# Kernel tuning notes

Hardware: AMD Instinct MI355X
Metric: run time of the kernel (lower is better)

## Reference

```python
import jax, jax.numpy as jnp
import numpy as np

B, S, H, NH, L, FF, V, T = 16, 256, 768, 12, 12, 3072, 30522, 9
DH = H // NH
LN_EPS = 1e-12


def _ln(x, g, b):
    m = jnp.mean(x, axis=-1, keepdims=True)
    v = jnp.mean((x - m) ** 2, axis=-1, keepdims=True)
    return (x - m) * jax.lax.rsqrt(v + LN_EPS) * g + b


def setup_inputs():
    key = jax.random.key(0)
    ks = jax.random.split(key, 20)
    n = lambda i, shape: jax.random.normal(ks[i], shape, jnp.float32) * 0.02
    lengths = jax.random.randint(ks[0], (B,), S // 2, S + 1)
    attention_mask = (jnp.arange(S)[None, :] < lengths[:, None]).astype(jnp.int32)
    return {
        "input_ids": jax.random.randint(ks[1], (B, S), 0, V),
        "attention_mask": attention_mask,
        "labels": jax.random.randint(ks[2], (B, S), 0, T),
        "word_emb": n(3, (V, H)),
        "pos_emb": n(4, (512, H)),
        "type_emb": n(5, (2, H)),
        "emb_g": jnp.ones((H,), jnp.float32), "emb_b": jnp.zeros((H,), jnp.float32),
        "lWq": n(6, (L, H, H)), "lbq": jnp.zeros((L, H), jnp.float32),
        "lWk": n(7, (L, H, H)), "lbk": jnp.zeros((L, H), jnp.float32),
        "lWv": n(8, (L, H, H)), "lbv": jnp.zeros((L, H), jnp.float32),
        "lWo": n(9, (L, H, H)), "lbo": jnp.zeros((L, H), jnp.float32),
        "lg1": jnp.ones((L, H), jnp.float32), "lb1": jnp.zeros((L, H), jnp.float32),
        "lWi": n(10, (L, H, FF)), "lbi": jnp.zeros((L, FF), jnp.float32),
        "lWf": n(11, (L, FF, H)), "lbf": jnp.zeros((L, H), jnp.float32),
        "lg2": jnp.ones((L, H), jnp.float32), "lb2": jnp.zeros((L, H), jnp.float32),
        "cls_W": n(12, (H, T)), "cls_b": jnp.zeros((T,), jnp.float32),
        "crf_start": jax.random.uniform(ks[13], (T,), jnp.float32, -0.1, 0.1),
        "crf_end": jax.random.uniform(ks[14], (T,), jnp.float32, -0.1, 0.1),
        "crf_trans": jax.random.uniform(ks[15], (T, T), jnp.float32, -0.1, 0.1),
    }


def _encoder(input_ids, attention_mask, word_emb, pos_emb, type_emb, emb_g, emb_b, layer_stack, cls_W, cls_b):
    x = word_emb[input_ids] + pos_emb[:S][None] + type_emb[0][None, None]  # [B,S,H]
    x = _ln(x, emb_g, emb_b)
    bias = (1.0 - attention_mask.astype(jnp.float32))[:, None, None, :] * -1e9  # [B,1,1,S]
    scale = 1.0 / np.sqrt(DH).astype(np.float32)

    def layer(h, p):
        Wq, bq, Wk, bk, Wv, bv, Wo, bo, g1, b1, Wi, bi, Wf, bf, g2, b2 = p
        q = (h @ Wq + bq).reshape(B, S, NH, DH)
        k = (h @ Wk + bk).reshape(B, S, NH, DH)
        v = (h @ Wv + bv).reshape(B, S, NH, DH)
        att = jax.nn.softmax(jnp.einsum('bqhd,bkhd->bhqk', q, k) * scale + bias, axis=-1)
        ctx = jnp.einsum('bhqk,bkhd->bqhd', att, v).reshape(B, S, H)
        h = _ln(h + ctx @ Wo + bo, g1, b1)
        ff = jax.nn.gelu(h @ Wi + bi, approximate=False) @ Wf + bf
        h = _ln(h + ff, g2, b2)
        return h, None

    x, _ = jax.lax.scan(layer, x, layer_stack)
    return x @ cls_W + cls_b  # [B,S,T]


def _crf_llh(em, tg, m, start, end, trans):
    # pytorch-crf forward, reduction='sum'. em [B,Lc,T], tg [B,Lc] int, m [B,Lc] bool
    mf = m.astype(em.dtype)
    em_sc = jnp.take_along_axis(em, tg[..., None], axis=-1)[..., 0]  # [B,Lc]
    tr_sc = trans[tg[:, :-1], tg[:, 1:]]                             # [B,Lc-1]
    num = start[tg[:, 0]] + em_sc[:, 0] + jnp.sum(mf[:, 1:] * (tr_sc + em_sc[:, 1:]), axis=1)
    seq_ends = jnp.sum(m.astype(jnp.int32), axis=1) - 1
    last_tag = jnp.take_along_axis(tg, seq_ends[:, None], axis=1)[:, 0]
    num = num + end[last_tag]

    def step(score, xs):
        em_t, m_t = xs
        nxt = jax.nn.logsumexp(score[:, :, None] + trans[None] + em_t[:, None, :], axis=1)
        return jnp.where(m_t[:, None], nxt, score), None

    score0 = start[None] + em[:, 0]
    score, _ = jax.lax.scan(step, score0, (em[:, 1:].transpose(1, 0, 2), m[:, 1:].transpose(1, 0)))
    den = jax.nn.logsumexp(score + end[None], axis=1)
    return jnp.sum(num - den)


def _viterbi(em, start, end, trans):
    # decode over the FULL sequence with all-ones mask (matches crf.decode(logits))
    def step(score, em_t):
        cand = score[:, :, None] + trans[None] + em_t[:, None, :]  # [B,T,T]
        return jnp.max(cand, axis=1), jnp.argmax(cand, axis=1)

    score0 = start[None] + em[:, 0]
    score, hist = jax.lax.scan(step, score0, em[:, 1:].transpose(1, 0, 2))  # hist [S-1,B,T]
    last = jnp.argmax(score + end[None], axis=1)  # [B]

    def back(tag, h):
        prev = jnp.take_along_axis(h, tag[:, None], axis=1)[:, 0]
        return prev, prev

    _, rev = jax.lax.scan(back, last, hist, reverse=True)  # rev[i] = tag at time i, i in [0,S-2]
    tags = jnp.concatenate([rev.transpose(1, 0), last[:, None]], axis=1)  # [B,S]
    return tags.astype(jnp.float32)


def reference(input_ids, attention_mask, labels, word_emb, pos_emb, type_emb, emb_g, emb_b,
              lWq, lbq, lWk, lbk, lWv, lbv, lWo, lbo, lg1, lb1, lWi, lbi, lWf, lbf, lg2, lb2,
              cls_W, cls_b, crf_start, crf_end, crf_trans):
    layer_stack = (lWq, lbq, lWk, lbk, lWv, lbv, lWo, lbo, lg1, lb1, lWi, lbi, lWf, lbf, lg2, lb2)
    logits = _encoder(input_ids, attention_mask, word_emb, pos_emb, type_emb, emb_g, emb_b, layer_stack, cls_W, cls_b)
    str_lens = jnp.sum(attention_mask, axis=-1)
    pos = jnp.arange(S)[None, :]
    mask = attention_mask.astype(bool) & (pos > 0) & (pos != (str_lens - 1)[:, None])
    tags_in = jnp.where(mask, labels, jnp.zeros_like(labels))
    loss = -_crf_llh(logits[:, 1:], tags_in[:, 1:], mask[:, 1:], crf_start, crf_end, crf_trans)
    tags = _viterbi(logits, crf_start, crf_end, crf_trans)
    return (loss, tags)
```

## Files before the change

### kernel.cpp

```cpp
#include <hip/hip_runtime.h>

#define B_ 16
#define S_ 256
#define H_ 768
#define NH_ 12
#define DH_ 64
#define L_ 12
#define FF_ 3072
#define T_ 9
#define NTOK (B_*S_)

typedef __attribute__((ext_vector_type(8))) short bfrag;
typedef __attribute__((ext_vector_type(8))) unsigned short us8;
typedef __attribute__((ext_vector_type(4))) float f4;

__device__ inline unsigned short f2bf(float x) {
    unsigned u = __builtin_bit_cast(unsigned, x);
    return (unsigned short)((u + 0x7fffu + ((u >> 16) & 1u)) >> 16);
}
__device__ inline float bf2f(unsigned short h) {
    unsigned u = ((unsigned)h) << 16;
    return __builtin_bit_cast(float, u);
}
__device__ inline void pack8(const float* v, us8& h, us8& l) {
    #pragma unroll
    for (int j = 0; j < 8; j++) {
        unsigned short hh = f2bf(v[j]);
        h[j] = hh;
        l[j] = f2bf(v[j] - bf2f(hh));
    }
}

__global__ __launch_bounds__(256) void k_conv_w(
    const float* __restrict__ Wq, const float* __restrict__ Wk,
    const float* __restrict__ Wv, const float* __restrict__ Wo,
    const float* __restrict__ Wi, const float* __restrict__ Wf,
    const float* __restrict__ bq, const float* __restrict__ bk, const float* __restrict__ bv,
    float* __restrict__ qkvbias, unsigned short* __restrict__ Wpk)
{
    int bid = blockIdx.x;
    int tid = threadIdx.x;
    if (bid == 0) {
        for (int i = tid; i < 3 * H_; i += 256)
            qkvbias[i] = (i < H_) ? bq[i] : (i < 2 * H_) ? bk[i - H_] : bv[i - 2 * H_];
    }
    const float* src; int Kd, Nd; size_t doff; int t;
    if (bid < 576)       { int m = bid / 144; src = (m == 0) ? Wq : (m == 1) ? Wk : (m == 2) ? Wv : Wo;
                           Kd = H_; Nd = H_; doff = (size_t)m * 73728; t = bid % 144; }
    else if (bid < 1152) { src = Wi; Kd = H_; Nd = FF_; doff = 294912; t = bid - 576; }
    else                 { src = Wf; Kd = FF_; Nd = H_; doff = 589824; t = bid - 1152; }
    int ntn = Nd / 64;
    int tk = t / ntn, tn = t % ntn;
    int k0 = tk * 64, n0 = tn * 64;
    __shared__ float tile[64][65];
    int r = tid >> 6, c = tid & 63;
    #pragma unroll
    for (int i = 0; i < 16; i++)
        tile[r + i * 4][c] = src[(size_t)(k0 + r + i * 4) * Nd + n0 + c];
    __syncthreads();
    #pragma unroll
    for (int e = 0; e < 2; e++) {
        int item = tid * 2 + e;
        int nl = item >> 3, kb = item & 7;
        float v8[8];
        #pragma unroll
        for (int j = 0; j < 8; j++) v8[j] = tile[kb * 8 + j][nl];
        us8 h, l; pack8(v8, h, l);
        unsigned short* p = Wpk + (doff + (size_t)(n0 + nl) * (Kd / 8) + (k0 / 8 + kb)) * 16;
        *reinterpret_cast<us8*>(p) = h;
        *reinterpret_cast<us8*>(p + 8) = l;
    }
}

__global__ __launch_bounds__(128) void k_embed_ln(
    const int* __restrict__ ids, const float* __restrict__ wemb,
    const float* __restrict__ pemb, const float* __restrict__ temb,
    const float* __restrict__ g, const float* __restrict__ bb,
    float* __restrict__ out, unsigned short* __restrict__ out_pk)
{
    int tok = blockIdx.x;
    int s = tok & (S_ - 1);
    int id = ids[tok];
    int tid = threadIdx.x;
    bool act = tid < 96;
    int idx = tid * 8;
    float v8[8];
    float sum = 0.f;
    if (act) {
        const float4* w4 = reinterpret_cast<const float4*>(wemb + (size_t)id * H_ + idx);
        const float4* p4 = reinterpret_cast<const float4*>(pemb + (size_t)s * H_ + idx);
        const float4* t4 = reinterpret_cast<const float4*>(temb + idx);
        #pragma unroll
        for (int q = 0; q < 2; q++) {
            float4 a = w4[q], b = p4[q], c = t4[q];
            v8[q*4+0] = a.x + b.x + c.x; v8[q*4+1] = a.y + b.y + c.y;
            v8[q*4+2] = a.z + b.z + c.z; v8[q*4+3] = a.w + b.w + c.w;
        }
        #pragma unroll
        for (int j = 0; j < 8; j++) sum += v8[j];
    }
    __shared__ float wsum[2], wvar[2];
    #pragma unroll
    for (int o = 32; o > 0; o >>= 1) sum += __shfl_xor(sum, o);
    if ((tid & 63) == 0) wsum[tid >> 6] = sum;
    __syncthreads();
    float mean = (wsum[0] + wsum[1]) * (1.0f / H_);
    float vs = 0.f;
    if (act) {
        for (int j = 0; j < 8; j++) { float d = v8[j] - mean; vs += d * d; }
    }
    #pragma unroll
    for (int o = 32; o > 0; o >>= 1) vs += __shfl_xor(vs, o);
    if ((tid & 63) == 0) wvar[tid >> 6] = vs;
    __syncthreads();
    float inv = 1.0f / sqrtf((wvar[0] + wvar[1]) * (1.0f / H_) + 1e-12f);
    if (act) {
        float o8[8];
        #pragma unroll
        for (int j = 0; j < 8; j++) o8[j] = (v8[j] - mean) * inv * g[idx + j] + bb[idx + j];
        float4* d4 = reinterpret_cast<float4*>(out + (size_t)tok * H_ + idx);
        d4[0] = make_float4(o8[0], o8[1], o8[2], o8[3]);
        d4[1] = make_float4(o8[4], o8[5], o8[6], o8[7]);
        us8 h, l; pack8(o8, h, l);
        unsigned short* p = out_pk + ((size_t)tok * 96 + tid) * 16;
        *reinterpret_cast<us8*>(p) = h;
        *reinterpret_cast<us8*>(p + 8) = l;
    }
}

__global__ __launch_bounds__(128) void k_res_ln(
    const float* __restrict__ x, const float* __restrict__ res,
    const float* __restrict__ g, const float* __restrict__ bb,
    float* __restrict__ out, unsigned short* __restrict__ out_pk)
{
    int tok = blockIdx.x;
    int tid = threadIdx.x;
    bool act = tid < 96;
    int idx = tid * 8;
    float v8[8];
    float sum = 0.f;
    if (act) {
        const float4* x4 = reinterpret_cast<const float4*>(x + (size_t)tok * H_ + idx);
        const float4* r4 = reinterpret_cast<const float4*>(res + (size_t)tok * H_ + idx);
        #pragma unroll
        for (int q = 0; q < 2; q++) {
            float4 a = x4[q], b = r4[q];
            v8[q*4+0] = a.x + b.x; v8[q*4+1] = a.y + b.y;
            v8[q*4+2] = a.z + b.z; v8[q*4+3] = a.w + b.w;
        }
        #pragma unroll
        for (int j = 0; j < 8; j++) sum += v8[j];
    }
    __shared__ float wsum[2], wvar[2];
    #pragma unroll
    for (int o = 32; o > 0; o >>= 1) sum += __shfl_xor(sum, o);
    if ((tid & 63) == 0) wsum[tid >> 6] = sum;
    __syncthreads();
    float mean = (wsum[0] + wsum[1]) * (1.0f / H_);
    float vs = 0.f;
    if (act) {
        for (int j = 0; j < 8; j++) { float d = v8[j] - mean; vs += d * d; }
    }
    #pragma unroll
    for (int o = 32; o > 0; o >>= 1) vs += __shfl_xor(vs, o);
    if ((tid & 63) == 0) wvar[tid >> 6] = vs;
    __syncthreads();
    float inv = 1.0f / sqrtf((wvar[0] + wvar[1]) * (1.0f / H_) + 1e-12f);
    if (act) {
        float o8[8];
        #pragma unroll
        for (int j = 0; j < 8; j++) o8[j] = (v8[j] - mean) * inv * g[idx + j] + bb[idx + j];
        float4* d4 = reinterpret_cast<float4*>(out + (size_t)tok * H_ + idx);
        d4[0] = make_float4(o8[0], o8[1], o8[2], o8[3]);
        d4[1] = make_float4(o8[4], o8[5], o8[6], o8[7]);
        us8 h, l; pack8(o8, h, l);
        unsigned short* p = out_pk + ((size_t)tok * 96 + tid) * 16;
        *reinterpret_cast<us8*>(p) = h;
        *reinterpret_cast<us8*>(p + 8) = l;
    }
}

__global__ __launch_bounds__(256) void k_gemm_pk(
    const unsigned short* __restrict__ A, const unsigned short* __restrict__ Wp,
    const float* __restrict__ bias,
    float* __restrict__ C0, float* __restrict__ C1, float* __restrict__ C2, int cpb,
    unsigned short* __restrict__ Cpk,
    int M, int N, int K, int act)
{
    __shared__ char smem[32768];
    char* smA = smem;
    char* smB = smem + 16384;

    int nbx = N >> 7;
    int nwg = (M >> 7) * nbx;
    int id = blockIdx.x;
    int cpx = nwg >> 3;
    int swz = (id & 7) * cpx + (id >> 3);
    int by = swz / nbx, bx = swz % nbx;
    int m0 = by << 7, n0 = bx << 7;
    int Kb = K >> 3;
    int nst = Kb >> 2;

    int tid = threadIdx.x;
    int lane = tid & 63, wid = tid >> 6;
    int wm = wid >> 1, wn = wid & 1;
    int fr = lane & 15, fq = lane >> 4;

    f4 acc[4][4];
    #pragma unroll
    for (int i = 0; i < 4; i++)
        #pragma unroll
        for (int j = 0; j < 4; j++) acc[i][j] = (f4){0.f, 0.f, 0.f, 0.f};

    const char* agp[4]; const char* bgp[4];
    int alds[4];
    #pragma unroll
    for (int i = 0; i < 4; i++) {
        int off = i * 4096 + tid * 16;
        int row = off >> 7, col = off & 127;
        agp[i] = (const char*)A + (size_t)(m0 + row) * (Kb * 32) + col;
        bgp[i] = (const char*)Wp + (size_t)(n0 + row) * (Kb * 32) + col;
        alds[i] = row * 128 + (col ^ ((row & 7) << 4));
    }

    int arow = wm * 64 + fr;
    int brow = wn * 64 + fr;
    int afo[4], bfo[4];
    #pragma unroll
    for (int mi = 0; mi < 4; mi++) {
        int r = arow + mi * 16;
        afo[mi] = r * 128 + ((fq * 32) ^ ((r & 7) << 4));
        int rb = brow + mi * 16;
        bfo[mi] = rb * 128 + ((fq * 32) ^ ((rb & 7) << 4));
    }

    us8 ra[4], rb[4];
    #pragma unroll
    for (int i = 0; i < 4; i++) {
        ra[i] = *reinterpret_cast<const us8*>(agp[i]);
        rb[i] = *reinterpret_cast<const us8*>(bgp[i]);
    }

    for (int ks = 0; ks < nst; ks++) {
        #pragma unroll
        for (int i = 0; i < 4; i++) {
            *reinterpret_cast<us8*>(smA + alds[i]) = ra[i];
            *reinterpret_cast<us8*>(smB + alds[i]) = rb[i];
        }
        __syncthreads();
        if (ks + 1 < nst) {
            #pragma unroll
            for (int i = 0; i < 4; i++) {
                ra[i] = *reinterpret_cast<const us8*>(agp[i] + (size_t)(ks + 1) * 128);
                rb[i] = *reinterpret_cast<const us8*>(bgp[i] + (size_t)(ks + 1) * 128);
            }
        }
        bfrag ah[4], al[4], bh[4], bl[4];
        #pragma unroll
        for (int mi = 0; mi < 4; mi++) {
            ah[mi] = *reinterpret_cast<const bfrag*>(smA + afo[mi]);
            al[mi] = *reinterpret_cast<const bfrag*>(smA + (afo[mi] ^ 16));
            bh[mi] = *reinterpret_cast<const bfrag*>(smB + bfo[mi]);
            bl[mi] = *reinterpret_cast<const bfrag*>(smB + (bfo[mi] ^ 16));
        }
        #pragma unroll
        for (int mi = 0; mi < 4; mi++) {
            #pragma unroll
            for (int ni = 0; ni < 4; ni++) {
                acc[mi][ni] = __builtin_amdgcn_mfma_f32_16x16x32_bf16(ah[mi], bh[ni], acc[mi][ni], 0, 0, 0);
                acc[mi][ni] = __builtin_amdgcn_mfma_f32_16x16x32_bf16(ah[mi], bl[ni], acc[mi][ni], 0, 0, 0);
                acc[mi][ni] = __builtin_amdgcn_mfma_f32_16x16x32_bf16(al[mi], bh[ni], acc[mi][ni], 0, 0, 0);
            }
        }
        __syncthreads();
    }

    if (act == 0) {
        #pragma unroll
        for (int mi = 0; mi < 4; mi++) {
            #pragma unroll
            for (int ni = 0; ni < 4; ni++) {
                int col = n0 + wn * 64 + ni * 16 + fr;
                float bv = bias[col];
                int buf = col / cpb;
                float* Cp = (buf == 0) ? C0 : (buf == 1) ? C1 : C2;
                int cc = col - buf * cpb;
                #pragma unroll
                for (int r = 0; r < 4; r++) {
                    int row = m0 + wm * 64 + mi * 16 + fq * 4 + r;
                    Cp[(size_t)row * cpb + cc] = acc[mi][ni][r] + bv;
                }
            }
        }
    } else {
        float* ebuf = (float*)smem;
        int Nb = N >> 3;
        #pragma unroll
        for (int mi = 0; mi < 4; mi++) {
            #pragma unroll
            for (int ni = 0; ni < 4; ni++) {
                int col = n0 + wn * 64 + ni * 16 + fr;
                float bv = bias[col];
                #pragma unroll
                for (int r = 0; r < 4; r++) {
                    float v = acc[mi][ni][r] + bv;
                    v = 0.5f * v * (1.0f + erff(v * 0.70710678118654752f));
                    ebuf[(wid * 16 + fq * 4 + r) * 68 + ni * 16 + fr] = v;
                }
            }
            #pragma unroll
            for (int e = 0; e < 2; e++) {
                int item = lane * 2 + e;
                int row16 = item >> 3, kb = item & 7;
                float v8[8];
                #pragma unroll
                for (int j = 0; j < 8; j++) v8[j] = ebuf[(wid * 16 + row16) * 68 + kb * 8 + j];
                us8 h, l; pack8(v8, h, l);
                int grow = m0 + wm * 64 + mi * 16 + row16;
                int gcb = ((n0 + wn * 64) >> 3) + kb;
                unsigned short* p = Cpk + ((size_t)grow * Nb + gcb) * 16;
                *reinterpret_cast<us8*>(p) = h;
                *reinterpret_cast<us8*>(p + 8) = l;
            }
        }
    }
}

#define SM_KH 0
#define SM_KL 5632
#define SM_VH 11264
#define SM_VL 16384
#define SM_PH 21504
#define SM_PL 26624
__global__ __launch_bounds__(256) void k_attn_fused(
    const float* __restrict__ Q, const float* __restrict__ Kb,
    const float* __restrict__ V, const int* __restrict__ amask,
    unsigned short* __restrict__ ctx_pk)
{
    __shared__ char smem[31744];
    unsigned short* KhS = (unsigned short*)(smem + SM_KH);
    unsigned short* KlS = (unsigned short*)(smem + SM_KL);
    unsigned short* VhS = (unsigned short*)(smem + SM_VH);
    unsigned short* VlS = (unsigned short*)(smem + SM_VL);
    unsigned short* PhS = (unsigned short*)(smem + SM_PH);
    unsigned short* PlS = (unsigned short*)(smem + SM_PL);

    int idx = blockIdx.x;
    int qt = idx & 3;
    int hd = (idx >> 2) % NH_;
    int b = idx / (4 * NH_);
    int tid = threadIdx.x;
    int lane = tid & 63, wid = tid >> 6;
    int fr = lane & 15, fq = lane >> 4;

    int q0 = qt * 64 + wid * 16;

    bfrag qh[2], ql[2];
    {
        const float* qbase = Q + ((size_t)(b * S_ + q0 + fr)) * H_ + hd * DH_;
        #pragma unroll
        for (int ks = 0; ks < 2; ks++) {
            const float4* p = reinterpret_cast<const float4*>(qbase + ks * 32 + fq * 8);
            float4 v0 = p[0], v1 = p[1];
            float vv[8] = {v0.x, v0.y, v0.z, v0.w, v1.x, v1.y, v1.z, v1.w};
            #pragma unroll
            for (int j = 0; j < 8; j++) {
                unsigned short h = f2bf(vv[j]);
                qh[ks][j] = (short)h;
                ql[ks][j] = (short)f2bf(vv[j] - bf2f(h));
            }
        }
    }

    f4 o[4];
    #pragma unroll
    for (int i = 0; i < 4; i++) o[i] = (f4){0.f, 0.f, 0.f, 0.f};
    float m[4], l[4];
    #pragma unroll
    for (int r = 0; r < 4; r++) { m[r] = -3e38f; l[r] = 0.f; }

    int kvrow = tid >> 3;
    int dbase = (tid & 7) * 8;

    for (int t = 0; t < 8; t++) {
        {
            const float* src = Kb + ((size_t)(b * S_ + t * 32 + kvrow)) * H_ + hd * DH_ + dbase;
            float4 a4 = reinterpret_cast<const float4*>(src)[0];
            float4 b4 = reinterpret_cast<const float4*>(src)[1];
            float vv[8] = {a4.x, a4.y, a4.z, a4.w, b4.x, b4.y, b4.z, b4.w};
            us8 h, l2;
            #pragma unroll
            for (int j = 0; j < 8; j++) {
                unsigned short hh = f2bf(vv[j]);
                h[j] = hh; l2[j] = f2bf(vv[j] - bf2f(hh));
            }
            *reinterpret_cast<us8*>(&KhS[kvrow * 88 + dbase]) = h;
            *reinterpret_cast<us8*>(&KlS[kvrow * 88 + dbase]) = l2;
        }
        {
            const float* src = V + ((size_t)(b * S_ + t * 32 + kvrow)) * H_ + hd * DH_ + dbase;
            float4 a4 = reinterpret_cast<const float4*>(src)[0];
            float4 b4 = reinterpret_cast<const float4*>(src)[1];
            float vv[8] = {a4.x, a4.y, a4.z, a4.w, b4.x, b4.y, b4.z, b4.w};
            #pragma unroll
            for (int j = 0; j < 8; j++) {
                unsigned short h = f2bf(vv[j]);
                VhS[(dbase + j) * 40 + kvrow] = h;
                VlS[(dbase + j) * 40 + kvrow] = f2bf(vv[j] - bf2f(h));
            }
        }
        __syncthreads();

        f4 s0 = (f4){0.f,0.f,0.f,0.f}, s1 = (f4){0.f,0.f,0.f,0.f};
        #pragma unroll
        for (int ks = 0; ks < 2; ks++) {
            bfrag kbh0 = *reinterpret_cast<const bfrag*>(&KhS[fr * 88 + ks * 32 + fq * 8]);
            bfrag kbl0 = *reinterpret_cast<const bfrag*>(&KlS[fr * 88 + ks * 32 + fq * 8]);
            bfrag kbh1 = *reinterpret_cast<const bfrag*>(&KhS[(16 + fr) * 88 + ks * 32 + fq * 8]);
            bfrag kbl1 = *reinterpret_cast<const bfrag*>(&KlS[(16 + fr) * 88 + ks * 32 + fq * 8]);
            s0 = __builtin_amdgcn_mfma_f32_16x16x32_bf16(qh[ks], kbh0, s0, 0, 0, 0);
            s0 = __builtin_amdgcn_mfma_f32_16x16x32_bf16(qh[ks], kbl0, s0, 0, 0, 0);
            s0 = __builtin_amdgcn_mfma_f32_16x16x32_bf16(ql[ks], kbh0, s0, 0, 0, 0);
            s1 = __builtin_amdgcn_mfma_f32_16x16x32_bf16(qh[ks], kbh1, s1, 0, 0, 0);
            s1 = __builtin_amdgcn_mfma_f32_16x16x32_bf16(qh[ks], kbl1, s1, 0, 0, 0);
            s1 = __builtin_amdgcn_mfma_f32_16x16x32_bf16(ql[ks], kbh1, s1, 0, 0, 0);
        }

        float cb0 = (amask[b * S_ + t * 32 + fr] == 0) ? -1e9f : 0.f;
        float cb1 = (amask[b * S_ + t * 32 + 16 + fr] == 0) ? -1e9f : 0.f;
        float sc0[4], sc1[4], fct[4], pr0[4], pr1[4];
        #pragma unroll
        for (int r = 0; r < 4; r++) {
            sc0[r] = s0[r] * 0.125f + cb0;
            sc1[r] = s1[r] * 0.125f + cb1;
            float tm = fmaxf(sc0[r], sc1[r]);
            #pragma unroll
            for (int od = 1; od < 16; od <<= 1) tm = fmaxf(tm, __shfl_xor(tm, od));
            float mn = fmaxf(m[r], tm);
            fct[r] = expf(m[r] - mn);
            pr0[r] = expf(sc0[r] - mn);
            pr1[r] = expf(sc1[r] - mn);
            float rs = pr0[r] + pr1[r];
            #pragma unroll
            for (int od = 1; od < 16; od <<= 1) rs += __shfl_xor(rs, od);
            l[r] = l[r] * fct[r] + rs;
            m[r] = mn;
        }
        #pragma unroll
        for (int ci = 0; ci < 4; ci++)
            #pragma unroll
            for (int r = 0; r < 4; r++) o[ci][r] *= fct[r];

        #pragma unroll
        for (int r = 0; r < 4; r++) {
            int row = fq * 4 + r;
            unsigned short h0 = f2bf(pr0[r]);
            PhS[wid * 640 + row * 40 + fr] = h0;
            PlS[wid * 640 + row * 40 + fr] = f2bf(pr0[r] - bf2f(h0));
            unsigned short h1 = f2bf(pr1[r]);
            PhS[wid * 640 + row * 40 + 16 + fr] = h1;
            PlS[wid * 640 + row * 40 + 16 + fr] = f2bf(pr1[r] - bf2f(h1));
        }

        bfrag pah = *reinterpret_cast<const bfrag*>(&PhS[wid * 640 + fr * 40 + fq * 8]);
        bfrag pal = *reinterpret_cast<const bfrag*>(&PlS[wid * 640 + fr * 40 + fq * 8]);
        #pragma unroll
        for (int ci = 0; ci < 4; ci++) {
            bfrag vbh = *reinterpret_cast<const bfrag*>(&VhS[(ci * 16 + fr) * 40 + fq * 8]);
            bfrag vbl = *reinterpret_cast<const bfrag*>(&VlS[(ci * 16 + fr) * 40 + fq * 8]);
            o[ci] = __builtin_amdgcn_mfma_f32_16x16x32_bf16(pah, vbh, o[ci], 0, 0, 0);
            o[ci] = __builtin_amdgcn_mfma_f32_16x16x32_bf16(pah, vbl, o[ci], 0, 0, 0);
            o[ci] = __builtin_amdgcn_mfma_f32_16x16x32_bf16(pal, vbh, o[ci], 0, 0, 0);
        }
        __syncthreads();
    }

    __syncthreads();
    float* eb = (float*)smem + wid * 1088;
    #pragma unroll
    for (int r = 0; r < 4; r++) {
        float inv = 1.0f / l[r];
        #pragma unroll
        for (int ci = 0; ci < 4; ci++)
            eb[(fq * 4 + r) * 68 + ci * 16 + fr] = o[ci][r] * inv;
    }
    __syncthreads();
    #pragma unroll
    for (int e = 0; e < 2; e++) {
        int item = lane * 2 + e;
        int row16 = item >> 3, kb = item & 7;
        float v8[8];
        #pragma unroll
        for (int j = 0; j < 8; j++) v8[j] = eb[row16 * 68 + kb * 8 + j];
        us8 h, l2; pack8(v8, h, l2);
        int grow = b * S_ + q0 + row16;
        int gcb = hd * 8 + kb;
        unsigned short* p = ctx_pk + ((size_t)grow * 96 + gcb) * 16;
        *reinterpret_cast<us8*>(p) = h;
        *reinterpret_cast<us8*>(p + 8) = l2;
    }
}

__global__ __launch_bounds__(64) void k_classifier(
    const float* __restrict__ Hs, const float* __restrict__ Wc,
    const float* __restrict__ bc, float* __restrict__ logits)
{
    int tok = blockIdx.x;
    int lane = threadIdx.x;
    const float* hr = Hs + (size_t)tok * H_;
    float acc[T_];
    #pragma unroll
    for (int j = 0; j < T_; j++) acc[j] = 0.f;
    for (int k = lane; k < H_; k += 64) {
        float hv = hr[k];
        const float* wr = Wc + (size_t)k * T_;
        #pragma unroll
        for (int j = 0; j < T_; j++) acc[j] = fmaf(hv, wr[j], acc[j]);
    }
    #pragma unroll
    for (int j = 0; j < T_; j++) {
        float v = acc[j];
        for (int o = 32; o > 0; o >>= 1) v += __shfl_down(v, o);
        if (lane == 0) logits[(size_t)tok * T_ + j] = v + bc[j];
    }
}

__global__ __launch_bounds__(256) void k_crf(
    const float* __restrict__ logits, const int* __restrict__ amask,
    const int* __restrict__ labels, const float* __restrict__ start,
    const float* __restrict__ endv, const float* __restrict__ trans,
    float* __restrict__ out_loss)
{
    __shared__ float res[B_];
    int tid = threadIdx.x;
    int lane = tid & 63;
    int g = lane >> 4;
    int bb = (tid >> 6) * 4 + g;
    int sj = lane & 15;
    int lb = lane & 48;

    int cnt = 0;
    for (int s = sj; s < S_; s += 16) cnt += amask[bb * S_ + s];
    #pragma unroll
    for (int o = 8; o > 0; o >>= 1) cnt += __shfl_xor(cnt, o);
    int len = cnt;

    float num = 0.f; int msum = 0;
    for (int s = 2 + sj; s < S_; s += 16) {
        int mk = (amask[bb * S_ + s] != 0) && (s != len - 1);
        if (mk) {
            int sp = s - 1;
            int mkp = (amask[bb * S_ + sp] != 0) && (sp != len - 1) && (sp > 0);
            int tp = mkp ? labels[bb * S_ + sp] : 0;
            int tc = labels[bb * S_ + s];
            num += trans[tp * T_ + tc] + logits[((size_t)(bb * S_ + s)) * T_ + tc];
            msum++;
        }
    }
    #pragma unroll
    for (int o = 8; o > 0; o >>= 1) { num += __shfl_xor(num, o); msum += __shfl_xor(msum, o); }
    int mk1 = (amask[bb * S_ + 1] != 0) && (1 != len - 1);
    msum += mk1 ? 1 : 0;
    int tg1 = mk1 ? labels[bb * S_ + 1] : 0;
    num += start[tg1] + logits[((size_t)(bb * S_ + 1)) * T_ + tg1];
    int ls = msum;
    int mkl = (amask[bb * S_ + ls] != 0) && (ls != len - 1) && (ls > 0);
    num += endv[mkl ? labels[bb * S_ + ls] : 0];

    float tc9[T_];
    #pragma unroll
    for (int i = 0; i < T_; i++) tc9[i] = 0.f;
    if (sj < T_) {
        #pragma unroll
        for (int i = 0; i < T_; i++) tc9[i] = trans[i * T_ + sj];
    }
    float score = (sj < T_) ? start[sj] + logits[((size_t)(bb * S_ + 1)) * T_ + sj] : 0.f;
    for (int s = 2; s < S_; s++) {
        float em = (sj < T_) ? logits[((size_t)(bb * S_ + s)) * T_ + sj] : 0.f;
        float si[T_];
        #pragma unroll
        for (int i = 0; i < T_; i++) si[i] = __shfl(score, lb + i);
        int mt = (amask[bb * S_ + s] != 0) && (s != len - 1);
        float mx = -1e30f;
        #pragma unroll
        for (int i = 0; i < T_; i++) mx = fmaxf(mx, si[i] + tc9[i]);
        float sum = 0.f;
        #pragma unroll
        for (int i = 0; i < T_; i++) sum += expf(si[i] + tc9[i] - mx);
        float nsc = mx + logf(sum) + em;
        if (mt) score = nsc;
    }

    float se = (sj < T_) ? score + endv[sj] : -1e30f;
    float fi[T_];
    #pragma unroll
    for (int i = 0; i < T_; i++) fi[i] = __shfl(se, lb + i);
    if (sj == 0) {
        float mx = -1e30f;
        #pragma unroll
        for (int i = 0; i < T_; i++) mx = fmaxf(mx, fi[i]);
        float sum = 0.f;
        #pragma unroll
        for (int i = 0; i < T_; i++) sum += expf(fi[i] - mx);
        res[bb] = (mx + logf(sum)) - num;
    }
    __syncthreads();
    if (tid == 0) {
        float tot = 0.f;
        #pragma unroll
        for (int i = 0; i < B_; i++) tot += res[i];
        out_loss[0] = tot;
    }
}

__global__ __launch_bounds__(64) void k_viterbi(
    const float* __restrict__ logits, const float* __restrict__ start,
    const float* __restrict__ endv, const float* __restrict__ trans,
    float* __restrict__ tags_out)
{
    int b = blockIdx.x;
    int j = threadIdx.x;
    __shared__ unsigned char hist[S_ - 1][T_];
    float tc9[T_];
    #pragma unroll
    for (int i = 0; i < T_; i++) tc9[i] = 0.f;
    if (j < T_) {
        #pragma unroll
        for (int i = 0; i < T_; i++) tc9[i] = trans[i * T_ + j];
    }
    float score = (j < T_) ? start[j] + logits[((size_t)(b * S_)) * T_ + j] : -1e30f;
    for (int t = 1; t < S_; t++) {
        float si[T_];
        #pragma unroll
        for (int i = 0; i < T_; i++) si[i] = __shfl(score, i);
        float best = -1e30f; int bi = 0;
        #pragma unroll
        for (int i = 0; i < T_; i++) {
            float c = si[i] + tc9[i];
            if (c > best) { best = c; bi = i; }
        }
        if (j < T_) {
            hist[t - 1][j] = (unsigned char)bi;
            score = best + logits[((size_t)(b * S_ + t)) * T_ + j];
        }
    }
    float se = (j < T_) ? score + endv[j] : -1e30f;
    float fi[T_];
    #pragma unroll
    for (int i = 0; i < T_; i++) fi[i] = __shfl(se, i);
    if (j == 0) {
        float best = -1e30f; int last = 0;
        #pragma unroll
        for (int i = 0; i < T_; i++) if (fi[i] > best) { best = fi[i]; last = i; }
        tags_out[b * S_ + (S_ - 1)] = (float)last;
        int cur = last;
        for (int t = S_ - 2; t >= 0; t--) {
            cur = hist[t][cur];
            tags_out[b * S_ + t] = (float)cur;
        }
    }
}

extern "C" void kernel_launch(void* const* d_in, const int* in_sizes, int n_in,
                              void* d_out, int out_size, void* d_ws, size_t ws_size,
                              hipStream_t stream)
{
    const int*   input_ids = (const int*)d_in[0];
    const int*   amask     = (const int*)d_in[1];
    const int*   labels    = (const int*)d_in[2];
    const float* word_emb  = (const float*)d_in[3];
    const float* pos_emb   = (const float*)d_in[4];
    const float* type_emb  = (const float*)d_in[5];
    const float* emb_g     = (const float*)d_in[6];
    const float* emb_b     = (const float*)d_in[7];
    const float* lWq = (const float*)d_in[8];
    const float* lbq = (const float*)d_in[9];
    const float* lWk = (const float*)d_in[10];
    const float* lbk = (const float*)d_in[11];
    const float* lWv = (const float*)d_in[12];
    const float* lbv = (const float*)d_in[13];
    const float* lWo = (const float*)d_in[14];
    const float* lbo = (const float*)d_in[15];
    const float* lg1 = (const float*)d_in[16];
    const float* lb1 = (const float*)d_in[17];
    const float* lWi = (const float*)d_in[18];
    const float* lbi = (const float*)d_in[19];
    const float* lWf = (const float*)d_in[20];
    const float* lbf = (const float*)d_in[21];
    const float* lg2 = (const float*)d_in[22];
    const float* lb2 = (const float*)d_in[23];
    const float* cls_W = (const float*)d_in[24];
    const float* cls_b = (const float*)d_in[25];
    const float* crf_start = (const float*)d_in[26];
    const float* crf_end   = (const float*)d_in[27];
    const float* crf_trans = (const float*)d_in[28];

    float* out = (float*)d_out;
    float* ws = (float*)d_ws;

    const size_t NH32 = (size_t)NTOK * H_;
    float* h       = ws;
    float* h_pk_f  = ws + NH32;
    float* q       = ws + 2 * NH32;
    float* kbuf    = ws + 3 * NH32;
    float* v       = ws + 4 * NH32;
    float* ctxpk_f = ws + 5 * NH32;
    float* tmp     = ws + 6 * NH32;
    float* Wpk_f   = ws + 7 * NH32;
    float* qkvbias = Wpk_f + 7077888;
    float* logits  = qkvbias + 3 * H_;

    unsigned short* h_pk   = (unsigned short*)h_pk_f;
    unsigned short* ctx_pk = (unsigned short*)ctxpk_f;
    unsigned short* Wpk    = (unsigned short*)Wpk_f;
    unsigned short* big_pk = (unsigned short*)q;

    k_embed_ln<<<NTOK, 128, 0, stream>>>(input_ids, word_emb, pos_emb, type_emb, emb_g, emb_b, h, h_pk);

    const size_t WOFF_O = 221184, WOFF_I = 294912, WOFF_F = 589824;

    for (int l = 0; l < L_; l++) {
        k_conv_w<<<1728, 256, 0, stream>>>(
            lWq + (size_t)l * H_ * H_, lWk + (size_t)l * H_ * H_,
            lWv + (size_t)l * H_ * H_, lWo + (size_t)l * H_ * H_,
            lWi + (size_t)l * H_ * FF_, lWf + (size_t)l * FF_ * H_,
            lbq + (size_t)l * H_, lbk + (size_t)l * H_, lbv + (size_t)l * H_,
            qkvbias, Wpk);

        k_gemm_pk<<<576, 256, 0, stream>>>(h_pk, Wpk, qkvbias,
            q, kbuf, v, H_, nullptr, NTOK, 3 * H_, H_, 0);

        k_attn_fused<<<B_ * NH_ * 4, 256, 0, stream>>>(q, kbuf, v, amask, ctx_pk);

        k_gemm_pk<<<192, 256, 0, stream>>>(ctx_pk, Wpk + WOFF_O * 16, lbo + (size_t)l * H_,
            tmp, tmp, tmp, H_, nullptr, NTOK, H_, H_, 0);

        k_res_ln<<<NTOK, 128, 0, stream>>>(tmp, h, lg1 + (size_t)l * H_, lb1 + (size_t)l * H_, h, h_pk);

        k_gemm_pk<<<768, 256, 0, stream>>>(h_pk, Wpk + WOFF_I * 16, lbi + (size_t)l * FF_,
            tmp, tmp, tmp, FF_, big_pk, NTOK, FF_, H_, 1);

        k_gemm_pk<<<192, 256, 0, stream>>>(big_pk, Wpk + WOFF_F * 16, lbf + (size_t)l * H_,
            tmp, tmp, tmp, H_, nullptr, NTOK, H_, FF_, 0);

        k_res_ln<<<NTOK, 128, 0, stream>>>(tmp, h, lg2 + (size_t)l * H_, lb2 + (size_t)l * H_, h, h_pk);
    }

    k_classifier<<<NTOK, 64, 0, stream>>>(h, cls_W, cls_b, logits);
    k_crf<<<1, 256, 0, stream>>>(logits, amask, labels, crf_start, crf_end, crf_trans, out);
    k_viterbi<<<B_, 64, 0, stream>>>(logits, crf_start, crf_end, crf_trans, out + 1);
}
```

Before: 4.163 ms.

## Use direct global-to-LDS loads in GEMM and fuse CRF with Viterbi kernel

The GEMM main loop now uses global_load_lds to copy A and B tiles straight into shared memory. The XOR swizzle moves to the global source addresses, so the register staging and manual LDS stores go away. The register prefetch of the next k-step is dropped, so loads are no longer overlapped with MFMA work across iterations. Separately, the CRF loss and Viterbi kernels are merged into one launch running in parallel blocks, with emission prefetch into registers and simplified mask logic in the forward recursion.

```diff
diff --git a/kernel.cpp b/kernel.cpp
--- a/kernel.cpp
+++ b/kernel.cpp
@@ -9,6 +9,9 @@
 #define FF_ 3072
 #define T_ 9
 #define NTOK (B_*S_)
+
+#define AS1 __attribute__((address_space(1)))
+#define AS3 __attribute__((address_space(3)))
 
 typedef __attribute__((ext_vector_type(8))) short bfrag;
 typedef __attribute__((ext_vector_type(8))) unsigned short us8;
@@ -190,6 +193,7 @@
     __shared__ char smem[32768];
     char* smA = smem;
     char* smB = smem + 16384;
+    unsigned smb = (unsigned)(size_t)(void*)smem;
 
     int nbx = N >> 7;
     int nwg = (M >> 7) * nbx;
@@ -200,6 +204,7 @@
     int m0 = by << 7, n0 = bx << 7;
     int Kb = K >> 3;
     int nst = Kb >> 2;
+    int rowbytes = Kb * 32;
 
     int tid = threadIdx.x;
     int lane = tid & 63, wid = tid >> 6;
@@ -213,48 +218,40 @@
         for (int j = 0; j < 4; j++) acc[i][j] = (f4){0.f, 0.f, 0.f, 0.f};
 
     const char* agp[4]; const char* bgp[4];
-    int alds[4];
     #pragma unroll
     for (int i = 0; i < 4; i++) {
-        int off = i * 4096 + tid * 16;
-        int row = off >> 7, col = off & 127;
-        agp[i] = (const char*)A + (size_t)(m0 + row) * (Kb * 32) + col;
-        bgp[i] = (const char*)Wp + (size_t)(n0 + row) * (Kb * 32) + col;
-        alds[i] = row * 128 + (col ^ ((row & 7) << 4));
-    }
-
-    int arow = wm * 64 + fr;
-    int brow = wn * 64 + fr;
+        int d = i * 4096 + tid * 16;
+        int row = d >> 7;
+        int colp = (d & 127) ^ ((row & 7) << 4);
+        agp[i] = (const char*)A + (size_t)(m0 + row) * rowbytes + colp;
+        bgp[i] = (const char*)Wp + (size_t)(n0 + row) * rowbytes + colp;
+    }
+
     int afo[4], bfo[4];
     #pragma unroll
     for (int mi = 0; mi < 4; mi++) {
-        int r = arow + mi * 16;
+        int r = wm * 64 + fr + mi * 16;
         afo[mi] = r * 128 + ((fq * 32) ^ ((r & 7) << 4));
-        int rb = brow + mi * 16;
+        int rb = wn * 64 + fr + mi * 16;
         bfo[mi] = rb * 128 + ((fq * 32) ^ ((rb & 7) << 4));
     }
 
-    us8 ra[4], rb[4];
-    #pragma unroll
-    for (int i = 0; i < 4; i++) {
-        ra[i] = *reinterpret_cast<const us8*>(agp[i]);
-        rb[i] = *reinterpret_cast<const us8*>(bgp[i]);
-    }
-
     for (int ks = 0; ks < nst; ks++) {
+        size_t ko = (size_t)ks * 128;
         #pragma unroll
         for (int i = 0; i < 4; i++) {
-            *reinterpret_cast<us8*>(smA + alds[i]) = ra[i];
-            *reinterpret_cast<us8*>(smB + alds[i]) = rb[i];
+            __builtin_amdgcn_global_load_lds((const AS1 void*)(size_t)(agp[i] + ko),
+                                             (AS3 void*)(unsigned)(smb + i * 4096 + wid * 1024),
+                                             16, 0, 0);
+        }
+        #pragma unroll
+        for (int i = 0; i < 4; i++) {
+            __builtin_amdgcn_global_load_lds((const AS1 void*)(size_t)(bgp[i] + ko),
+                                             (AS3 void*)(unsigned)(smb + 16384 + i * 4096 + wid * 1024),
+                                             16, 0, 0);
         }
         __syncthreads();
-        if (ks + 1 < nst) {
-            #pragma unroll
-            for (int i = 0; i < 4; i++) {
-                ra[i] = *reinterpret_cast<const us8*>(agp[i] + (size_t)(ks + 1) * 128);
-                rb[i] = *reinterpret_cast<const us8*>(bgp[i] + (size_t)(ks + 1) * 128);
-            }
-        }
+
         bfrag ah[4], al[4], bh[4], bl[4];
         #pragma unroll
         for (int mi = 0; mi < 4; mi++) {
@@ -525,138 +522,142 @@
     }
 }
 
-__global__ __launch_bounds__(256) void k_crf(
+__global__ __launch_bounds__(256) void k_crf_vit(
     const float* __restrict__ logits, const int* __restrict__ amask,
     const int* __restrict__ labels, const float* __restrict__ start,
     const float* __restrict__ endv, const float* __restrict__ trans,
-    float* __restrict__ out_loss)
+    float* __restrict__ out)
 {
-    __shared__ float res[B_];
+    int blk = blockIdx.x;
     int tid = threadIdx.x;
-    int lane = tid & 63;
-    int g = lane >> 4;
-    int bb = (tid >> 6) * 4 + g;
-    int sj = lane & 15;
-    int lb = lane & 48;
-
-    int cnt = 0;
-    for (int s = sj; s < S_; s += 16) cnt += amask[bb * S_ + s];
-    #pragma unroll
-    for (int o = 8; o > 0; o >>= 1) cnt += __shfl_xor(cnt, o);
-    int len = cnt;
-
-    float num = 0.f; int msum = 0;
-    for (int s = 2 + sj; s < S_; s += 16) {
-        int mk = (amask[bb * S_ + s] != 0) && (s != len - 1);
-        if (mk) {
-            int sp = s - 1;
-            int mkp = (amask[bb * S_ + sp] != 0) && (sp != len - 1) && (sp > 0);
-            int tp = mkp ? labels[bb * S_ + sp] : 0;
-            int tc = labels[bb * S_ + s];
-            num += trans[tp * T_ + tc] + logits[((size_t)(bb * S_ + s)) * T_ + tc];
-            msum++;
-        }
-    }
-    #pragma unroll
-    for (int o = 8; o > 0; o >>= 1) { num += __shfl_xor(num, o); msum += __shfl_xor(msum, o); }
-    int mk1 = (amask[bb * S_ + 1] != 0) && (1 != len - 1);
-    msum += mk1 ? 1 : 0;
-    int tg1 = mk1 ? labels[bb * S_ + 1] : 0;
-    num += start[tg1] + logits[((size_t)(bb * S_ + 1)) * T_ + tg1];
-    int ls = msum;
-    int mkl = (amask[bb * S_ + ls] != 0) && (ls != len - 1) && (ls > 0);
-    num += endv[mkl ? labels[bb * S_ + ls] : 0];
-
-    float tc9[T_];
-    #pragma unroll
-    for (int i = 0; i < T_; i++) tc9[i] = 0.f;
-    if (sj < T_) {
-        #pragma unroll
-        for (int i = 0; i < T_; i++) tc9[i] = trans[i * T_ + sj];
-    }
-    float score = (sj < T_) ? start[sj] + logits[((size_t)(bb * S_ + 1)) * T_ + sj] : 0.f;
-    for (int s = 2; s < S_; s++) {
-        float em = (sj < T_) ? logits[((size_t)(bb * S_ + s)) * T_ + sj] : 0.f;
-        float si[T_];
-        #pragma unroll
-        for (int i = 0; i < T_; i++) si[i] = __shfl(score, lb + i);
-        int mt = (amask[bb * S_ + s] != 0) && (s != len - 1);
-        float mx = -1e30f;
-        #pragma unroll
-        for (int i = 0; i < T_; i++) mx = fmaxf(mx, si[i] + tc9[i]);
-        float sum = 0.f;
-        #pragma unroll
-        for (int i = 0; i < T_; i++) sum += expf(si[i] + tc9[i] - mx);
-        float nsc = mx + logf(sum) + em;
-        if (mt) score = nsc;
-    }
-
-    float se = (sj < T_) ? score + endv[sj] : -1e30f;
-    float fi[T_];
-    #pragma unroll
-    for (int i = 0; i < T_; i++) fi[i] = __shfl(se, lb + i);
-    if (sj == 0) {
-        float mx = -1e30f;
-        #pragma unroll
-        for (int i = 0; i < T_; i++) mx = fmaxf(mx, fi[i]);
-        float sum = 0.f;
-        #pragma unroll
-        for (int i = 0; i < T_; i++) sum += expf(fi[i] - mx);
-        res[bb] = (mx + logf(sum)) - num;
-    }
-    __syncthreads();
-    if (tid == 0) {
-        float tot = 0.f;
-        #pragma unroll
-        for (int i = 0; i < B_; i++) tot += res[i];
-        out_loss[0] = tot;
-    }
-}
-
-__global__ __launch_bounds__(64) void k_viterbi(
-    const float* __restrict__ logits, const float* __restrict__ start,
-    const float* __restrict__ endv, const float* __restrict__ trans,
-    float* __restrict__ tags_out)
-{
-    int b = blockIdx.x;
-    int j = threadIdx.x;
-    __shared__ unsigned char hist[S_ - 1][T_];
-    float tc9[T_];
-    #pragma unroll
-    for (int i = 0; i < T_; i++) tc9[i] = 0.f;
-    if (j < T_) {
-        #pragma unroll
-        for (int i = 0; i < T_; i++) tc9[i] = trans[i * T_ + j];
-    }
-    float score = (j < T_) ? start[j] + logits[((size_t)(b * S_)) * T_ + j] : -1e30f;
-    for (int t = 1; t < S_; t++) {
-        float si[T_];
-        #pragma unroll
-        for (int i = 0; i < T_; i++) si[i] = __shfl(score, i);
-        float best = -1e30f; int bi = 0;
-        #pragma unroll
-        for (int i = 0; i < T_; i++) {
-            float c = si[i] + tc9[i];
-            if (c > best) { best = c; bi = i; }
-        }
-        if (j < T_) {
-            hist[t - 1][j] = (unsigned char)bi;
-            score = best + logits[((size_t)(b * S_ + t)) * T_ + j];
-        }
-    }
-    float se = (j < T_) ? score + endv[j] : -1e30f;
-    float fi[T_];
-    #pragma unroll
-    for (int i = 0; i < T_; i++) fi[i] = __shfl(se, i);
-    if (j == 0) {
-        float best = -1e30f; int last = 0;
-        #pragma unroll
-        for (int i = 0; i < T_; i++) if (fi[i] > best) { best = fi[i]; last = i; }
-        tags_out[b * S_ + (S_ - 1)] = (float)last;
-        int cur = last;
-        for (int t = S_ - 2; t >= 0; t--) {
-            cur = hist[t][cur];
-            tags_out[b * S_ + t] = (float)cur;
+    if (blk == 0) {
+        __shared__ float res[B_];
+        int lane = tid & 63;
+        int bb = (tid >> 6) * 4 + (lane >> 4);
+        int sj = lane & 15;
+        int lb = lane & 48;
+
+        int cnt = 0;
+        for (int s = sj; s < S_; s += 16) cnt += amask[bb * S_ + s];
+        #pragma unroll
+        for (int o = 8; o > 0; o >>= 1) cnt += __shfl_xor(cnt, o);
+        int len = cnt;
+        int lim = len - 1;
+
+        float num = 0.f;
+        for (int s = 2 + sj; s < S_; s += 16) {
+            if (s < lim) {
+                int tp = labels[bb * S_ + s - 1];
+                int tc = labels[bb * S_ + s];
+                num += trans[tp * T_ + tc] + logits[((size_t)(bb * S_ + s)) * T_ + tc];
+            }
+        }
+        #pragma unroll
+        for (int o = 8; o > 0; o >>= 1) num += __shfl_xor(num, o);
+        int tg1 = labels[bb * S_ + 1];
+        num += start[tg1] + logits[((size_t)(bb * S_ + 1)) * T_ + tg1];
+        num += endv[labels[bb * S_ + (len - 2)]];
+
+        float tc9[T_];
+        #pragma unroll
+        for (int i = 0; i < T_; i++) tc9[i] = (sj < T_) ? trans[i * T_ + sj] : 0.f;
+        float score = (sj < T_) ? start[sj] + logits[((size_t)(bb * S_ + 1)) * T_ + sj] : 0.f;
+        const float* embase = logits + (size_t)bb * S_ * T_ + sj;
+        float emb[8];
+        #pragma unroll
+        for (int c = 0; c < 8; c++) emb[c] = (sj < T_) ? embase[(2 + c) * T_] : 0.f;
+        for (int s0 = 2; s0 < S_; s0 += 8) {
+            #pragma unroll
+            for (int c = 0; c < 8; c++) {
+                int s = s0 + c;
+                if (s < S_) {
+                    float em = emb[c];
+                    emb[c] = (sj < T_ && s + 8 < S_) ? embase[(size_t)(s + 8) * T_] : 0.f;
+                    float si[T_];
+                    #pragma unroll
+                    for (int i = 0; i < T_; i++) si[i] = __shfl(score, lb + i);
+                    float mx = -1e30f;
+                    #pragma unroll
+                    for (int i = 0; i < T_; i++) mx = fmaxf(mx, si[i] + tc9[i]);
+                    float sum = 0.f;
+                    #pragma unroll
+                    for (int i = 0; i < T_; i++) sum += expf(si[i] + tc9[i] - mx);
+                    float nsc = mx + logf(sum) + em;
+                    if (s < lim) score = nsc;
+                }
+            }
+        }
+        float se = (sj < T_) ? score + endv[sj] : -1e30f;
+        float fi[T_];
+        #pragma unroll
+        for (int i = 0; i < T_; i++) fi[i] = __shfl(se, lb + i);
+        if (sj == 0) {
+            float mx = -1e30f;
+            #pragma unroll
+            for (int i = 0; i < T_; i++) mx = fmaxf(mx, fi[i]);
+            float sum = 0.f;
+            #pragma unroll
+            for (int i = 0; i < T_; i++) sum += expf(fi[i] - mx);
+            res[bb] = (mx + logf(sum)) - num;
+        }
+        __syncthreads();
+        if (tid == 0) {
+            float tot = 0.f;
+            #pragma unroll
+            for (int i = 0; i < B_; i++) tot += res[i];
+            out[0] = tot;
+        }
+    } else {
+        if (tid >= 64) return;
+        int b = blk - 1;
+        int j = tid;
+        float* tags_out = out + 1;
+        __shared__ unsigned char hist[S_ - 1][T_];
+        float tc9[T_];
+        #pragma unroll
+        for (int i = 0; i < T_; i++) tc9[i] = (j < T_) ? trans[i * T_ + j] : 0.f;
+        float score = (j < T_) ? start[j] + logits[((size_t)(b * S_)) * T_ + j] : -1e30f;
+        const float* embase = logits + (size_t)b * S_ * T_ + j;
+        float emb[8];
+        #pragma unroll
+        for (int c = 0; c < 8; c++) emb[c] = (j < T_) ? embase[(1 + c) * T_] : 0.f;
+        for (int t0 = 1; t0 < S_; t0 += 8) {
+            #pragma unroll
+            for (int c = 0; c < 8; c++) {
+                int t = t0 + c;
+                if (t < S_) {
+                    float em = emb[c];
+                    emb[c] = (j < T_ && t + 8 < S_) ? embase[(size_t)(t + 8) * T_] : 0.f;
+                    float si[T_];
+                    #pragma unroll
+                    for (int i = 0; i < T_; i++) si[i] = __shfl(score, i);
+                    float best = -1e30f; int bi = 0;
+                    #pragma unroll
+                    for (int i = 0; i < T_; i++) {
+                        float cv = si[i] + tc9[i];
+                        if (cv > best) { best = cv; bi = i; }
+                    }
+                    if (j < T_) {
+                        hist[t - 1][j] = (unsigned char)bi;
+                        score = best + em;
+                    }
+                }
+            }
+        }
+        float se = (j < T_) ? score + endv[j] : -1e30f;
+        float fi[T_];
+        #pragma unroll
+        for (int i = 0; i < T_; i++) fi[i] = __shfl(se, i);
+        if (j == 0) {
+            float best = -1e30f; int last = 0;
+            #pragma unroll
+            for (int i = 0; i < T_; i++) if (fi[i] > best) { best = fi[i]; last = i; }
+            tags_out[b * S_ + (S_ - 1)] = (float)last;
+            int cur = last;
+            for (int t = S_ - 2; t >= 0; t--) {
+                cur = hist[t][cur];
+                tags_out[b * S_ + t] = (float)cur;
+            }
         }
     }
 }
@@ -747,6 +748,5 @@
     }
 
     k_classifier<<<NTOK, 64, 0, stream>>>(h, cls_W, cls_b, logits);
-    k_crf<<<1, 256, 0, stream>>>(logits, amask, labels, crf_start, crf_end, crf_trans, out);
-    k_viterbi<<<B_, 64, 0, stream>>>(logits, crf_start, crf_end, crf_trans, out + 1);
-}
+    k_crf_vit<<<1 + B_, 256, 0, stream>>>(logits, amask, labels, crf_start, crf_end, crf_trans, out);
+}
```

Result: slower. 4.642 ms (+11.5%).
